# Optimization experiments

Measured on AMD Instinct MI355X. Metric: run time of the kernel, lower is better.

The kernel has to match this reference:

```python
import jax, jax.numpy as jnp
import numpy as np

B, S, H, R = 4, 4096, 768, 242
HK = H // 3  # k/v/attn-output feature dim (256)
THETA = 10000.0


def _rope_table(seq_len, dim, theta=THETA):
    # Reproduces LlamaRotaryEmbedding.forward: returns [seq_len, dim] = cat(sin, cos)
    pos = jnp.arange(seq_len, dtype=jnp.float32)
    freqs = theta ** (-jnp.arange(0, dim, 2, dtype=jnp.float32) / dim)  # [dim/2]
    ang = pos[:, None] * freqs[None, :]  # [S, dim/2]
    return jnp.concatenate([jnp.sin(ang), jnp.cos(ang)], axis=-1)  # [S, dim]


def setup_inputs() -> dict:
    key = jax.random.key(0)
    ks = jax.random.split(key, 9)
    init = lambda k, shape: (jax.random.normal(k, shape, dtype=jnp.float32) * 0.02)
    return {
        "x": jax.random.normal(ks[0], (B, S, H), dtype=jnp.float32),
        # torch nn.Linear weights have shape [out_features, in_features]; y = x @ W.T
        "q_low": init(ks[1], (R, H)),  "q_high": init(ks[2], (H, R)),
        "k_low": init(ks[3], (R, H)),  "k_high": init(ks[4], (HK, R)),
        "v_low": init(ks[5], (R, H)),  "v_high": init(ks[6], (HK, R)),
        "o_low": init(ks[7], (R, HK)), "o_high": init(ks[8], (H, R)),
    }


def reference(x, q_low, q_high, k_low, k_high, v_low, v_high, o_low, o_high):
    b, s, h = x.shape
    # NOTE: in the original module, rope_emb(q) / rope_emb(k) discard the projected
    # q/k values and return the same [S, H] sin/cos position table, so q_proj/k_proj
    # are dead code (XLA will DCE them). We keep only the live computation.
    v = (x @ v_low.T) @ v_high.T  # [B, S, HK] factorized v projection
    t = _rope_table(s, h)         # q = k = t, shape [S, H]
    attn = jax.nn.softmax(t @ t.T, axis=-1)  # [S, S], input-independent
    ctx = jnp.einsum('st,btd->bsd', attn, v)  # [B, S, HK]
    return (ctx @ o_low.T) @ o_high.T         # [B, S, H]
```

## Files before the change

### kernel.cpp

```cpp
#include <hip/hip_runtime.h>
#include <hip/hip_bf16.h>


typedef __bf16 bf16x8 __attribute__((ext_vector_type(8)));
typedef float  f32x4  __attribute__((ext_vector_type(4)));

#define GLD16(g, l) __builtin_amdgcn_global_load_lds(                         \
    (const __attribute__((address_space(1))) void*)(g),                       \
    (__attribute__((address_space(3))) void*)(l), 16, 0, 0)


__global__ __launch_bounds__(256) void prep_ptvlt(const float* __restrict__ vh,
                                                  const float* __restrict__ ol,
                                                  const float* __restrict__ vl,
                                                  float* __restrict__ pt,
                                                  __bf16* __restrict__ vlt) {
    if (blockIdx.x < 242) {
        int j = blockIdx.x, i = threadIdx.x;
        float s = 0.f;
        if (i < 242) {
            for (int k = 0; k < 256; ++k)
                s += vh[k * 242 + i] * ol[j * 256 + k];
        }
        pt[j * 256 + i] = s;
    } else {
        int n = (blockIdx.x - 242) * 256 + threadIdx.x;
        int i = n >> 8, r = n & 255;
        vlt[n] = (r < 242) ? (__bf16)vl[r * 768 + i] : (__bf16)0.f;
    }
}

__global__ __launch_bounds__(256) void prep_q(const float* __restrict__ pt,
                                              const float* __restrict__ oh,
                                              __bf16* __restrict__ qb) {
    int j = blockIdx.x, r = threadIdx.x;
    float s = 0.f;
    for (int k = 0; k < 242; ++k)
        s += pt[k * 256 + r] * oh[j * 242 + k];
    qb[j * 256 + r] = (__bf16)s;
}

__global__ __launch_bounds__(256, 2) void gemm_nt_w(const __bf16* __restrict__ A,
                                                    const __bf16* __restrict__ Bt,
                                                    __bf16* __restrict__ C,
                                                    int Ndim, int Kdim) {
    __shared__ alignas(16) __bf16 lA[128 * 32];
    __shared__ alignas(16) __bf16 lB[128 * 32];

    const int tid  = threadIdx.x;
    const int wave = tid >> 6, lane = tid & 63;
    const int quad = lane >> 4, l16 = lane & 15;
    const int wm = (wave >> 1) * 64, wn = (wave & 1) * 64;

    const __bf16* Ab = A + (long)blockIdx.x * 128 * Kdim;
    const __bf16* Bb = Bt + (long)blockIdx.y * 128 * Kdim;

    f32x4 acc[4][4] = {};

    for (int k0 = 0; k0 < Kdim; k0 += 32) {
#pragma unroll
        for (int it = 0; it < 2; ++it) {
            int cb = it * 256 + wave * 64;
            int c  = cb + lane;
            GLD16(Ab + (long)(c >> 2) * Kdim + k0 + (c & 3) * 8, &lA[cb * 8]);
            GLD16(Bb + (long)(c >> 2) * Kdim + k0 + (c & 3) * 8, &lB[cb * 8]);
        }
        __syncthreads();

        bf16x8 af[4], bfr[4];
#pragma unroll
        for (int i = 0; i < 4; ++i)
            af[i] = *(const bf16x8*)&lA[(wm + i * 16 + l16) * 32 + quad * 8];
#pragma unroll
        for (int i = 0; i < 4; ++i)
            bfr[i] = *(const bf16x8*)&lB[(wn + i * 16 + l16) * 32 + quad * 8];

#pragma unroll
        for (int mi = 0; mi < 4; ++mi)
#pragma unroll
            for (int ni = 0; ni < 4; ++ni)
                acc[mi][ni] = __builtin_amdgcn_mfma_f32_16x16x32_bf16(
                    af[mi], bfr[ni], acc[mi][ni], 0, 0, 0);

        __syncthreads();
    }

    const long rbase = (long)blockIdx.x * 128 + wm + quad * 4;
    const long cbase = (long)blockIdx.y * 128 + wn + l16;
#pragma unroll
    for (int mi = 0; mi < 4; ++mi)
#pragma unroll
        for (int ni = 0; ni < 4; ++ni)
#pragma unroll
            for (int j = 0; j < 4; ++j)
                C[(rbase + mi * 16 + j) * Ndim + cbase + ni * 16] =
                    (__bf16)acc[mi][ni][j];
}

__global__ __launch_bounds__(512, 2) void gemm_xw(const float* __restrict__ A,
                                                  const __bf16* __restrict__ Bt,
                                                  float* __restrict__ C) {
    __shared__ __bf16 lA[2][64 * 72];

    const int tid  = threadIdx.x;
    const int wave = tid >> 6, lane = tid & 63;
    const int quad = lane >> 4, l16 = lane & 15;

    const int mt = blockIdx.x;
    const float* Ab = A + (long)mt * 64 * 768;

    const int srow = tid >> 3, scol = (tid & 7) * 8;
    const float* ga = Ab + srow * 768 + scol;

    const int nb = wave * 96;
    const __bf16* Bw = Bt + (long)(nb + l16) * 768 + quad * 8;

    f32x4 acc[6][4] = {};
    bf16x8 bcur[6][2], bnxt[6][2];

    f32x4 a0 = *(const f32x4*)(ga);
    f32x4 a1 = *(const f32x4*)(ga + 4);
#pragma unroll
    for (int g = 0; g < 6; ++g)
#pragma unroll
        for (int kf = 0; kf < 2; ++kf)
            bcur[g][kf] = *(const bf16x8*)(Bw + (long)g * 16 * 768 + kf * 32);
    {
        bf16x8 h = { (__bf16)a0[0], (__bf16)a0[1], (__bf16)a0[2], (__bf16)a0[3],
                     (__bf16)a1[0], (__bf16)a1[1], (__bf16)a1[2], (__bf16)a1[3] };
        *(bf16x8*)&lA[0][srow * 72 + scol] = h;
    }
    __syncthreads();

#pragma unroll
    for (int c = 0; c < 12; ++c) {
        const int cur = c & 1, nxt = cur ^ 1;
        const int koff = (c + 1) * 64;

        if (c < 11) {
            a0 = *(const f32x4*)(ga + koff);
            a1 = *(const f32x4*)(ga + koff + 4);
#pragma unroll
            for (int g = 0; g < 6; ++g)
#pragma unroll
                for (int kf = 0; kf < 2; ++kf)
                    bnxt[g][kf] = *(const bf16x8*)(Bw + (long)g * 16 * 768 +
                                                   koff + kf * 32);
        }

#pragma unroll
        for (int kf = 0; kf < 2; ++kf) {
            bf16x8 af[4];
#pragma unroll
            for (int m = 0; m < 4; ++m)
                af[m] = *(const bf16x8*)
                        &lA[cur][(m * 16 + l16) * 72 + kf * 32 + quad * 8];
#pragma unroll
            for (int g = 0; g < 6; ++g)
#pragma unroll
                for (int m = 0; m < 4; ++m)
                    acc[g][m] = __builtin_amdgcn_mfma_f32_16x16x32_bf16(
                        af[m], bcur[g][kf], acc[g][m], 0, 0, 0);
        }

        if (c < 11) {
            bf16x8 h = { (__bf16)a0[0], (__bf16)a0[1], (__bf16)a0[2], (__bf16)a0[3],
                         (__bf16)a1[0], (__bf16)a1[1], (__bf16)a1[2], (__bf16)a1[3] };
            *(bf16x8*)&lA[nxt][srow * 72 + scol] = h;
#pragma unroll
            for (int g = 0; g < 6; ++g)
#pragma unroll
                for (int kf = 0; kf < 2; ++kf)
                    bcur[g][kf] = bnxt[g][kf];
            __syncthreads();
        }
    }

    const long rb = (long)mt * 64 + quad * 4;
    const int  cb = nb + l16;
#pragma unroll
    for (int g = 0; g < 6; ++g)
#pragma unroll
        for (int m = 0; m < 4; ++m)
#pragma unroll
            for (int j = 0; j < 4; ++j)
                C[(rb + m * 16 + j) * 768 + cb + g * 16] = acc[g][m][j];
}


extern "C" void kernel_launch(void* const* d_in, const int* in_sizes, int n_in,
                              void* d_out, int out_size, void* d_ws, size_t ws_size,
                              hipStream_t stream) {
    const float* x      = (const float*)d_in[0];
    const float* v_low  = (const float*)d_in[5];
    const float* v_high = (const float*)d_in[6];
    const float* o_low  = (const float*)d_in[7];
    const float* o_high = (const float*)d_in[8];
    float* out = (float*)d_out;

    char* ws = (char*)d_ws;
    float*  pt  = (float*) (ws + 0);
    __bf16* qb  = (__bf16*)(ws + 262144);
    __bf16* vlt = (__bf16*)(ws + 655360);
    __bf16* wtb = (__bf16*)(ws + 1048576);

    prep_ptvlt<<<1010, 256, 0, stream>>>(v_high, o_low, v_low, pt, vlt);
    prep_q    <<<768,  256, 0, stream>>>(pt, o_high, qb);

    gemm_nt_w<<<dim3(6, 6), 256, 0, stream>>>(qb, vlt, wtb, 768, 256);

    gemm_xw<<<256, 512, 0, stream>>>(x, wtb, out);
}
```

Before: 172.3 us.

## Store W in MFMA fragment-packed layout and shrink gemm_nt_w tiles

gemm_nt_w now writes its output directly in the per-lane fragment order that gemm_xw consumes. Each wave in gemm_xw can then load its B fragments as contiguous 512-element chunks instead of strided row reads. gemm_nt_w tiles shrink from 128 to 64 so the grid grows from 36 to 144 blocks, with occupancy hint 4, and the small prep loops get unroll pragmas. The fragment-packed store is scattered, and the layout logic now ties the two kernels tightly together.

```diff
diff --git a/kernel.cpp b/kernel.cpp
--- a/kernel.cpp
+++ b/kernel.cpp
@@ -19,6 +19,7 @@
         int j = blockIdx.x, i = threadIdx.x;
         float s = 0.f;
         if (i < 242) {
+#pragma unroll 32
             for (int k = 0; k < 256; ++k)
                 s += vh[k * 242 + i] * ol[j * 256 + k];
         }
@@ -35,66 +36,65 @@
                                               __bf16* __restrict__ qb) {
     int j = blockIdx.x, r = threadIdx.x;
     float s = 0.f;
+#pragma unroll 32
     for (int k = 0; k < 242; ++k)
         s += pt[k * 256 + r] * oh[j * 242 + k];
     qb[j * 256 + r] = (__bf16)s;
 }
 
-__global__ __launch_bounds__(256, 2) void gemm_nt_w(const __bf16* __restrict__ A,
+__global__ __launch_bounds__(256, 4) void gemm_nt_w(const __bf16* __restrict__ A,
                                                     const __bf16* __restrict__ Bt,
                                                     __bf16* __restrict__ C,
-                                                    int Ndim, int Kdim) {
-    __shared__ alignas(16) __bf16 lA[128 * 32];
-    __shared__ alignas(16) __bf16 lB[128 * 32];
+                                                    int Kdim) {
+    __shared__ alignas(16) __bf16 lA[64 * 32];
+    __shared__ alignas(16) __bf16 lB[64 * 32];
 
     const int tid  = threadIdx.x;
     const int wave = tid >> 6, lane = tid & 63;
     const int quad = lane >> 4, l16 = lane & 15;
-    const int wm = (wave >> 1) * 64, wn = (wave & 1) * 64;
-
-    const __bf16* Ab = A + (long)blockIdx.x * 128 * Kdim;
-    const __bf16* Bb = Bt + (long)blockIdx.y * 128 * Kdim;
-
-    f32x4 acc[4][4] = {};
+    const int wm = (wave >> 1) * 32, wn = (wave & 1) * 32;
+
+    const __bf16* Ab = A + (long)blockIdx.x * 64 * Kdim;
+    const __bf16* Bb = Bt + (long)blockIdx.y * 64 * Kdim;
+
+    f32x4 acc[2][2] = {};
 
     for (int k0 = 0; k0 < Kdim; k0 += 32) {
-#pragma unroll
-        for (int it = 0; it < 2; ++it) {
-            int cb = it * 256 + wave * 64;
-            int c  = cb + lane;
-            GLD16(Ab + (long)(c >> 2) * Kdim + k0 + (c & 3) * 8, &lA[cb * 8]);
-            GLD16(Bb + (long)(c >> 2) * Kdim + k0 + (c & 3) * 8, &lB[cb * 8]);
-        }
+        GLD16(Ab + (long)(tid >> 2) * Kdim + k0 + (tid & 3) * 8, &lA[wave * 512]);
+        GLD16(Bb + (long)(tid >> 2) * Kdim + k0 + (tid & 3) * 8, &lB[wave * 512]);
         __syncthreads();
 
-        bf16x8 af[4], bfr[4];
-#pragma unroll
-        for (int i = 0; i < 4; ++i)
-            af[i] = *(const bf16x8*)&lA[(wm + i * 16 + l16) * 32 + quad * 8];
-#pragma unroll
-        for (int i = 0; i < 4; ++i)
+        bf16x8 af[2], bfr[2];
+#pragma unroll
+        for (int i = 0; i < 2; ++i) {
+            af[i]  = *(const bf16x8*)&lA[(wm + i * 16 + l16) * 32 + quad * 8];
             bfr[i] = *(const bf16x8*)&lB[(wn + i * 16 + l16) * 32 + quad * 8];
-
-#pragma unroll
-        for (int mi = 0; mi < 4; ++mi)
-#pragma unroll
-            for (int ni = 0; ni < 4; ++ni)
+        }
+#pragma unroll
+        for (int mi = 0; mi < 2; ++mi)
+#pragma unroll
+            for (int ni = 0; ni < 2; ++ni)
                 acc[mi][ni] = __builtin_amdgcn_mfma_f32_16x16x32_bf16(
                     af[mi], bfr[ni], acc[mi][ni], 0, 0, 0);
-
         __syncthreads();
     }
 
-    const long rbase = (long)blockIdx.x * 128 + wm + quad * 4;
-    const long cbase = (long)blockIdx.y * 128 + wn + l16;
-#pragma unroll
-    for (int mi = 0; mi < 4; ++mi)
-#pragma unroll
-        for (int ni = 0; ni < 4; ++ni)
-#pragma unroll
-            for (int j = 0; j < 4; ++j)
-                C[(rbase + mi * 16 + j) * Ndim + cbase + ni * 16] =
+    const int rb = blockIdx.x * 64 + wm + quad * 4;
+    const int ib = blockIdx.y * 64 + wn + l16;
+#pragma unroll
+    for (int mi = 0; mi < 2; ++mi)
+#pragma unroll
+        for (int ni = 0; ni < 2; ++ni) {
+            const int i  = ib + ni * 16;
+            const int kc = i >> 5, qi = (i >> 3) & 3, e = i & 7;
+#pragma unroll
+            for (int j = 0; j < 4; ++j) {
+                const int r = rb + mi * 16 + j;
+                const int g = r >> 4, lr = r & 15;
+                C[((g * 24 + kc) * 64 + qi * 16 + lr) * 8 + e] =
                     (__bf16)acc[mi][ni][j];
+            }
+        }
 }
 
 __global__ __launch_bounds__(512, 2) void gemm_xw(const float* __restrict__ A,
@@ -113,7 +113,7 @@
     const float* ga = Ab + srow * 768 + scol;
 
     const int nb = wave * 96;
-    const __bf16* Bw = Bt + (long)(nb + l16) * 768 + quad * 8;
+    const __bf16* Bw = Bt + (long)wave * 6 * 24 * 512 + lane * 8;
 
     f32x4 acc[6][4] = {};
     bf16x8 bcur[6][2], bnxt[6][2];
@@ -124,7 +124,7 @@
     for (int g = 0; g < 6; ++g)
 #pragma unroll
         for (int kf = 0; kf < 2; ++kf)
-            bcur[g][kf] = *(const bf16x8*)(Bw + (long)g * 16 * 768 + kf * 32);
+            bcur[g][kf] = *(const bf16x8*)(Bw + ((g * 24 + kf) << 9));
     {
         bf16x8 h = { (__bf16)a0[0], (__bf16)a0[1], (__bf16)a0[2], (__bf16)a0[3],
                      (__bf16)a1[0], (__bf16)a1[1], (__bf16)a1[2], (__bf16)a1[3] };
@@ -144,8 +144,8 @@
             for (int g = 0; g < 6; ++g)
 #pragma unroll
                 for (int kf = 0; kf < 2; ++kf)
-                    bnxt[g][kf] = *(const bf16x8*)(Bw + (long)g * 16 * 768 +
-                                                   koff + kf * 32);
+                    bnxt[g][kf] = *(const bf16x8*)
+                        (Bw + ((g * 24 + (c + 1) * 2 + kf) << 9));
         }
 
 #pragma unroll
@@ -207,7 +207,7 @@
     prep_ptvlt<<<1010, 256, 0, stream>>>(v_high, o_low, v_low, pt, vlt);
     prep_q    <<<768,  256, 0, stream>>>(pt, o_high, qb);
 
-    gemm_nt_w<<<dim3(6, 6), 256, 0, stream>>>(qb, vlt, wtb, 768, 256);
+    gemm_nt_w<<<dim3(12, 12), 256, 0, stream>>>(qb, vlt, wtb, 256);
 
     gemm_xw<<<256, 512, 0, stream>>>(x, wtb, out);
 }
```

Result: faster. 149.3 us (-13.3%).
